# Kernel tuning notes

Hardware: AMD Instinct MI355X
Metric: run time of the kernel (lower is better)

The kernel has to match this reference:

```python
import jax, jax.numpy as jnp
import numpy as np

SQRT_D_K = 64 ** 0.5  # d_model ** 0.5 from __init__
NEG_INF = -1e9


def setup_inputs() -> dict:
    key = jax.random.key(0)
    kq, kk, kv, kp = jax.random.split(key, 4)
    B, H, S, Dh = 4, 16, 2048, 64
    q = jax.random.normal(kq, (B, H, S, Dh), dtype=jnp.float32)
    k = jax.random.normal(kk, (B, H, S, Dh), dtype=jnp.float32)
    v = jax.random.normal(kv, (B, H, S, Dh), dtype=jnp.float32)
    # causal mask: 1 above the diagonal (positions to mask), [1,1,S,S]
    casual_mask = jnp.triu(jnp.ones((S, S), dtype=jnp.int32), k=1)[None, None]
    # padding mask: 1 marks padded tokens, [B,S]
    padding_mask = jax.random.randint(kp, (B, S), 0, 2, dtype=jnp.int32)
    return {"q": q, "k": k, "v": v, "casual_mask": casual_mask,
            "padding_mask": padding_mask}


def reference(q, k, v, casual_mask, padding_mask):
    # score: [B,H,S,S]
    score = jnp.einsum("bhqd,bhkd->bhqk", q, k) / SQRT_D_K
    score = jnp.where(casual_mask == 1, NEG_INF, score)
    score = jnp.where(padding_mask[:, None, None, :] == 1, NEG_INF, score)
    attn_weights = jax.nn.softmax(score, axis=-1)
    # dropout p=0.0 (eval) -> identity
    attention_output = jnp.einsum("bhqk,bhkd->bhqd", attn_weights, v)
    return attention_output, attn_weights
```

## Files before the change

kernel.cpp:

```cpp
#include <hip/hip_runtime.h>
#include <hip/hip_bf16.h>

#define S_LEN 2048
#define DH    64
#define QT    128
#define KT    64
#define NW    4

typedef __attribute__((ext_vector_type(8))) short bf16x8;
typedef __attribute__((ext_vector_type(4))) float f32x4;
typedef __attribute__((ext_vector_type(4))) unsigned u32x4;
typedef __attribute__((ext_vector_type(2))) unsigned u32x2;

static __device__ __forceinline__ unsigned cvtpk(float a, float b) {
    unsigned r;
    asm("v_cvt_pk_bf16_f32 %0, %1, %2" : "=v"(r) : "v"(a), "v"(b));
    return r;
}

__global__ __launch_bounds__(256) void attn_main(
    const float* __restrict__ Q, const float* __restrict__ K,
    const float* __restrict__ V, const int* __restrict__ PAD,
    float* __restrict__ OUT, float* __restrict__ W)
{
    __shared__ short Kt[KT][72];
    __shared__ short VT[DH][72];
    __shared__ short Pb[NW][16][72];
    __shared__ float sinv[2][NW][16];
    __shared__ unsigned long long padm[32];

    const int orig = blockIdx.x;
    const int wg   = (orig & 7) * 128 + (orig >> 3);
    const int bh   = wg >> 4;
    const int qt   = 15 - (wg & 15);
    const int b    = bh >> 4;
    const int q0   = qt * QT;

    const int tid  = threadIdx.x;
    const int wv   = tid >> 6;
    const int l    = tid & 63;
    const int lr   = l & 15;
    const int lg   = l >> 4;
    const int k2   = (tid & 31) * 2;
    const int dblk = (tid >> 5) * 8;

    const size_t hoff = (size_t)bh * S_LEN * DH;
    const float* Qh = Q + hoff;
    const float* Kh = K + hoff;
    const float* Vh = V + hoff;
    float* Oh = OUT + hoff;
    float* Wh = W + (size_t)bh * S_LEN * S_LEN;

    const int nkt    = 2 * qt + 2;
    const int ktmaxA = 2 * qt;

    for (int i = tid; i < S_LEN; i += 256) {
        unsigned long long m = __ballot(PAD[b * S_LEN + i] != 0);
        if (l == 0) padm[i >> 6] = m;
    }

    bf16x8 qfA[2], qfB[2];
    #pragma unroll
    for (int blk = 0; blk < 2; ++blk) {
        const float* qp = Qh + (size_t)(q0 + blk * 64 + wv * 16 + lr) * DH + lg * 8;
        #pragma unroll
        for (int h = 0; h < 2; ++h) {
            f32x4 a  = *reinterpret_cast<const f32x4*>(qp + h * 32);
            f32x4 b4 = *reinterpret_cast<const f32x4*>(qp + h * 32 + 4);
            u32x4 t;
            t[0] = cvtpk(a[0] * 0.125f,  a[1] * 0.125f);
            t[1] = cvtpk(a[2] * 0.125f,  a[3] * 0.125f);
            t[2] = cvtpk(b4[0] * 0.125f, b4[1] * 0.125f);
            t[3] = cvtpk(b4[2] * 0.125f, b4[3] * 0.125f);
            (blk ? qfB[h] : qfA[h]) = __builtin_bit_cast(bf16x8, t);
        }
    }

    const f32x4 z4 = {0.f, 0.f, 0.f, 0.f};
    f32x4 accA[4] = {z4, z4, z4, z4};
    f32x4 accB[4] = {z4, z4, z4, z4};
    float rsA = 0.f, rsB = 0.f;
    const int qcolA = q0 + wv * 16 + lr;
    const int qcolB = qcolA + 64;

    auto ablock = [&](const bf16x8 (&qf)[2], const int qcol, float& rsref,
                      f32x4 (&accb)[4], const unsigned long long pm, const int ktbase) {
        f32x4 sc[4] = {z4, z4, z4, z4};
        #pragma unroll
        for (int s = 0; s < 4; ++s)
            #pragma unroll
            for (int h = 0; h < 2; ++h) {
                bf16x8 kf = *reinterpret_cast<const bf16x8*>(&Kt[s * 16 + lr][h * 32 + lg * 8]);
                sc[s] = __builtin_amdgcn_mfma_f32_16x16x32_bf16(kf, qf[h], sc[s], 0, 0, 0);
            }
        #pragma unroll
        for (int s = 0; s < 4; ++s) {
            const int kbase = ktbase + s * 16 + lg * 4;
            float e[4];
            #pragma unroll
            for (int r = 0; r < 4; ++r) {
                const bool padded = (pm >> (s * 16 + lg * 4 + r)) & 1ull;
                const bool ok = (kbase + r <= qcol) && !padded;
                e[r] = ok ? __expf(sc[s][r]) : 0.f;
                rsref += e[r];
            }
            u32x2 p2 = { cvtpk(e[0], e[1]), cvtpk(e[2], e[3]) };
            *reinterpret_cast<u32x2*>(&Pb[wv][lr][s * 16 + lg * 4]) = p2;
        }
        #pragma unroll
        for (int kk = 0; kk < 2; ++kk) {
            bf16x8 pf = *reinterpret_cast<const bf16x8*>(&Pb[wv][lr][kk * 32 + lg * 8]);
            #pragma unroll
            for (int dt = 0; dt < 4; ++dt) {
                bf16x8 vf = *reinterpret_cast<const bf16x8*>(&VT[dt * 16 + lr][kk * 32 + lg * 8]);
                accb[dt] = __builtin_amdgcn_mfma_f32_16x16x32_bf16(pf, vf, accb[dt], 0, 0, 0);
            }
        }
    };

    for (int kt = 0; kt < nkt; ++kt) {
        __syncthreads();
        {
            const float* kp = Kh + ((size_t)(kt * KT) + l) * DH + wv * 16;
            f32x4 pk0 = *reinterpret_cast<const f32x4*>(kp);
            f32x4 pk1 = *reinterpret_cast<const f32x4*>(kp + 4);
            f32x4 pk2 = *reinterpret_cast<const f32x4*>(kp + 8);
            f32x4 pk3 = *reinterpret_cast<const f32x4*>(kp + 12);
            const float* vp = Vh + ((size_t)(kt * KT) + k2) * DH + dblk;
            f32x4 pva0 = *reinterpret_cast<const f32x4*>(vp);
            f32x4 pva1 = *reinterpret_cast<const f32x4*>(vp + 4);
            f32x4 pvb0 = *reinterpret_cast<const f32x4*>(vp + DH);
            f32x4 pvb1 = *reinterpret_cast<const f32x4*>(vp + DH + 4);
            u32x4 ta, tb;
            ta[0] = cvtpk(pk0[0], pk0[1]); ta[1] = cvtpk(pk0[2], pk0[3]);
            ta[2] = cvtpk(pk1[0], pk1[1]); ta[3] = cvtpk(pk1[2], pk1[3]);
            tb[0] = cvtpk(pk2[0], pk2[1]); tb[1] = cvtpk(pk2[2], pk2[3]);
            tb[2] = cvtpk(pk3[0], pk3[1]); tb[3] = cvtpk(pk3[2], pk3[3]);
            *reinterpret_cast<u32x4*>(&Kt[l][wv * 16])     = ta;
            *reinterpret_cast<u32x4*>(&Kt[l][wv * 16 + 8]) = tb;
            #pragma unroll
            for (int j = 0; j < 4; ++j)
                *reinterpret_cast<unsigned*>(&VT[dblk + j][k2])     = cvtpk(pva0[j], pvb0[j]);
            #pragma unroll
            for (int j = 0; j < 4; ++j)
                *reinterpret_cast<unsigned*>(&VT[dblk + 4 + j][k2]) = cvtpk(pva1[j], pvb1[j]);
        }
        __syncthreads();

        const unsigned long long pm = padm[kt];
        if (kt <= ktmaxA) ablock(qfA, qcolA, rsA, accA, pm, kt * KT);
        ablock(qfB, qcolB, rsB, accB, pm, kt * KT);

        #pragma unroll 1
        for (int row = kt; row < QT; row += nkt) {
            const int kend = q0 + (row < 64 ? 64 : 128);
            const int n4 = (S_LEN - kend) >> 2;
            f32x4* dst = reinterpret_cast<f32x4*>(Wh + (size_t)(q0 + row) * S_LEN + kend);
            for (int i = tid; i < n4; i += 256)
                __builtin_nontemporal_store(z4, dst + i);
        }
    }

    rsA += __shfl_xor(rsA, 16, 64); rsA += __shfl_xor(rsA, 32, 64);
    rsB += __shfl_xor(rsB, 16, 64); rsB += __shfl_xor(rsB, 32, 64);
    const float invA = rsA > 0.f ? 1.f / rsA : 0.f;
    const float invB = rsB > 0.f ? 1.f / rsB : 0.f;

    if (lg == 0) { sinv[0][wv][lr] = invA; sinv[1][wv][lr] = invB; }
    float inv4A[4], inv4B[4];
    #pragma unroll
    for (int r = 0; r < 4; ++r) {
        inv4A[r] = sinv[0][wv][lg * 4 + r];
        inv4B[r] = sinv[1][wv][lg * 4 + r];
    }

    const int qa = q0 + wv * 16 + lg * 4;
    #pragma unroll
    for (int dt = 0; dt < 4; ++dt)
        #pragma unroll
        for (int r = 0; r < 4; ++r) {
            Oh[(size_t)(qa + r) * DH + dt * 16 + lr]      = accA[dt][r] * inv4A[r];
            Oh[(size_t)(qa + 64 + r) * DH + dt * 16 + lr] = accB[dt][r] * inv4B[r];
        }

    auto wblock = [&](const bf16x8 (&qf)[2], const int qcol, const float inv,
                      const unsigned long long pm, const int ktbase) {
        f32x4 sc[4] = {z4, z4, z4, z4};
        #pragma unroll
        for (int s = 0; s < 4; ++s)
            #pragma unroll
            for (int h = 0; h < 2; ++h) {
                bf16x8 kf = *reinterpret_cast<const bf16x8*>(&Kt[s * 16 + lr][h * 32 + lg * 8]);
                sc[s] = __builtin_amdgcn_mfma_f32_16x16x32_bf16(kf, qf[h], sc[s], 0, 0, 0);
            }
        #pragma unroll
        for (int s = 0; s < 4; ++s) {
            const int kbase = ktbase + s * 16 + lg * 4;
            f32x4 t;
            #pragma unroll
            for (int r = 0; r < 4; ++r) {
                const bool padded = (pm >> (s * 16 + lg * 4 + r)) & 1ull;
                const bool ok = (kbase + r <= qcol) && !padded;
                t[r] = ok ? __expf(sc[s][r]) * inv : 0.f;
            }
            __builtin_nontemporal_store(t,
                reinterpret_cast<f32x4*>(Wh + (size_t)qcol * S_LEN + kbase));
        }
    };

    for (int kt = 0; kt < nkt; ++kt) {
        __syncthreads();
        {
            const float* kp = Kh + ((size_t)(kt * KT) + l) * DH + wv * 16;
            f32x4 pk0 = *reinterpret_cast<const f32x4*>(kp);
            f32x4 pk1 = *reinterpret_cast<const f32x4*>(kp + 4);
            f32x4 pk2 = *reinterpret_cast<const f32x4*>(kp + 8);
            f32x4 pk3 = *reinterpret_cast<const f32x4*>(kp + 12);
            u32x4 ta, tb;
            ta[0] = cvtpk(pk0[0], pk0[1]); ta[1] = cvtpk(pk0[2], pk0[3]);
            ta[2] = cvtpk(pk1[0], pk1[1]); ta[3] = cvtpk(pk1[2], pk1[3]);
            tb[0] = cvtpk(pk2[0], pk2[1]); tb[1] = cvtpk(pk2[2], pk2[3]);
            tb[2] = cvtpk(pk3[0], pk3[1]); tb[3] = cvtpk(pk3[2], pk3[3]);
            *reinterpret_cast<u32x4*>(&Kt[l][wv * 16])     = ta;
            *reinterpret_cast<u32x4*>(&Kt[l][wv * 16 + 8]) = tb;
        }
        __syncthreads();

        const unsigned long long pm = padm[kt];
        if (kt <= ktmaxA) wblock(qfA, qcolA, invA, pm, kt * KT);
        wblock(qfB, qcolB, invB, pm, kt * KT);
    }
}

__global__ __launch_bounds__(256) void attn_fixup(
    const int* __restrict__ PAD, const float* __restrict__ V,
    float* __restrict__ OUT, float* __restrict__ W)
{
    const int bh = blockIdx.x;
    const int b  = bh >> 4;
    const int tid = threadIdx.x;
    __shared__ int red;
    __shared__ float tmp[256];
    __shared__ float vs[DH];
    if (tid == 0) red = S_LEN;
    __syncthreads();
    int m = S_LEN;
    for (int i = tid; i < S_LEN; i += 256)
        if (PAD[b * S_LEN + i] == 0) m = min(m, i);
    atomicMin(&red, m);
    __syncthreads();
    const int fz = red;
    if (fz == 0) return;

    const float* Vh = V + (size_t)bh * S_LEN * DH;
    float a = 0.f;
    const int dcol = tid & 63, part = tid >> 6;
    for (int kk = part; kk < S_LEN; kk += 4) a += Vh[(size_t)kk * DH + dcol];
    tmp[tid] = a;
    __syncthreads();
    if (tid < DH)
        vs[tid] = (tmp[tid] + tmp[tid + 64] + tmp[tid + 128] + tmp[tid + 192]) * (1.f / S_LEN);
    __syncthreads();

    float* Wh = W + (size_t)bh * S_LEN * S_LEN;
    float* Oh = OUT + (size_t)bh * S_LEN * DH;
    const f32x4 u = {1.f / S_LEN, 1.f / S_LEN, 1.f / S_LEN, 1.f / S_LEN};
    for (int qa2 = 0; qa2 < fz; ++qa2) {
        f32x4* dst = reinterpret_cast<f32x4*>(Wh + (size_t)qa2 * S_LEN);
        for (int i = tid; i < S_LEN / 4; i += 256) dst[i] = u;
        if (tid < DH) Oh[(size_t)qa2 * DH + tid] = vs[tid];
    }
}

extern "C" void kernel_launch(void* const* d_in, const int* in_sizes, int n_in,
                              void* d_out, int out_size, void* d_ws, size_t ws_size,
                              hipStream_t stream) {
    const float* q   = (const float*)d_in[0];
    const float* k   = (const float*)d_in[1];
    const float* v   = (const float*)d_in[2];
    const int*   pad = (const int*)d_in[4];

    float* out = (float*)d_out;
    float* w   = out + (size_t)4 * 16 * S_LEN * DH;

    attn_main<<<dim3(64 * 16), dim3(256), 0, stream>>>(q, k, v, pad, out, w);
    attn_fixup<<<dim3(64), dim3(256), 0, stream>>>(pad, v, out, w);
}
```

Before: 470.5 us.

## Split attention into rowsum kernel and fused PV-plus-weights kernel

Splits the single kernel into two launches. The first computes QK^T, the masked exp row sums and their inverses, and zero-fills the masked region of the weight matrix, writing the inverses to the workspace. The second recomputes scores and writes the normalized weights while it accumulates P·V in the same pass. This drops the separate second K pass inside one block and the V work from the rowsum stage, at the cost of an extra kernel launch and global round-trips for the inverse sums.

```diff
diff --git a/kernel.cpp b/kernel.cpp
--- a/kernel.cpp
+++ b/kernel.cpp
@@ -18,15 +18,12 @@
     return r;
 }
 
-__global__ __launch_bounds__(256) void attn_main(
+
+__global__ __launch_bounds__(256) void attn_rowsum(
     const float* __restrict__ Q, const float* __restrict__ K,
-    const float* __restrict__ V, const int* __restrict__ PAD,
-    float* __restrict__ OUT, float* __restrict__ W)
+    const int* __restrict__ PAD, float* __restrict__ W, float* __restrict__ INV)
 {
     __shared__ short Kt[KT][72];
-    __shared__ short VT[DH][72];
-    __shared__ short Pb[NW][16][72];
-    __shared__ float sinv[2][NW][16];
     __shared__ unsigned long long padm[32];
 
     const int orig = blockIdx.x;
@@ -36,19 +33,15 @@
     const int b    = bh >> 4;
     const int q0   = qt * QT;
 
-    const int tid  = threadIdx.x;
-    const int wv   = tid >> 6;
-    const int l    = tid & 63;
-    const int lr   = l & 15;
-    const int lg   = l >> 4;
-    const int k2   = (tid & 31) * 2;
-    const int dblk = (tid >> 5) * 8;
+    const int tid = threadIdx.x;
+    const int wv  = tid >> 6;
+    const int l   = tid & 63;
+    const int lr  = l & 15;
+    const int lg  = l >> 4;
 
     const size_t hoff = (size_t)bh * S_LEN * DH;
     const float* Qh = Q + hoff;
     const float* Kh = K + hoff;
-    const float* Vh = V + hoff;
-    float* Oh = OUT + hoff;
     float* Wh = W + (size_t)bh * S_LEN * S_LEN;
 
     const int nkt    = 2 * qt + 2;
@@ -77,14 +70,12 @@
     }
 
     const f32x4 z4 = {0.f, 0.f, 0.f, 0.f};
-    f32x4 accA[4] = {z4, z4, z4, z4};
-    f32x4 accB[4] = {z4, z4, z4, z4};
     float rsA = 0.f, rsB = 0.f;
     const int qcolA = q0 + wv * 16 + lr;
     const int qcolB = qcolA + 64;
 
-    auto ablock = [&](const bf16x8 (&qf)[2], const int qcol, float& rsref,
-                      f32x4 (&accb)[4], const unsigned long long pm, const int ktbase) {
+    auto rblock = [&](const bf16x8 (&qf)[2], const int qcol, float& rsref,
+                      const unsigned long long pm, const int ktbase) {
         f32x4 sc[4] = {z4, z4, z4, z4};
         #pragma unroll
         for (int s = 0; s < 4; ++s)
@@ -96,14 +87,144 @@
         #pragma unroll
         for (int s = 0; s < 4; ++s) {
             const int kbase = ktbase + s * 16 + lg * 4;
+            #pragma unroll
+            for (int r = 0; r < 4; ++r) {
+                const bool padded = (pm >> (s * 16 + lg * 4 + r)) & 1ull;
+                const bool ok = (kbase + r <= qcol) && !padded;
+                rsref += ok ? __expf(sc[s][r]) : 0.f;
+            }
+        }
+    };
+
+    for (int kt = 0; kt < nkt; ++kt) {
+        __syncthreads();
+        {
+            const float* kp = Kh + ((size_t)(kt * KT) + l) * DH + wv * 16;
+            f32x4 pk0 = *reinterpret_cast<const f32x4*>(kp);
+            f32x4 pk1 = *reinterpret_cast<const f32x4*>(kp + 4);
+            f32x4 pk2 = *reinterpret_cast<const f32x4*>(kp + 8);
+            f32x4 pk3 = *reinterpret_cast<const f32x4*>(kp + 12);
+            u32x4 ta, tb;
+            ta[0] = cvtpk(pk0[0], pk0[1]); ta[1] = cvtpk(pk0[2], pk0[3]);
+            ta[2] = cvtpk(pk1[0], pk1[1]); ta[3] = cvtpk(pk1[2], pk1[3]);
+            tb[0] = cvtpk(pk2[0], pk2[1]); tb[1] = cvtpk(pk2[2], pk2[3]);
+            tb[2] = cvtpk(pk3[0], pk3[1]); tb[3] = cvtpk(pk3[2], pk3[3]);
+            *reinterpret_cast<u32x4*>(&Kt[l][wv * 16])     = ta;
+            *reinterpret_cast<u32x4*>(&Kt[l][wv * 16 + 8]) = tb;
+        }
+        __syncthreads();
+
+        const unsigned long long pm = padm[kt];
+        if (kt <= ktmaxA) rblock(qfA, qcolA, rsA, pm, kt * KT);
+        rblock(qfB, qcolB, rsB, pm, kt * KT);
+
+        #pragma unroll 1
+        for (int row = kt; row < QT; row += nkt) {
+            const int kend = q0 + (row < 64 ? 64 : 128);
+            const int n4 = (S_LEN - kend) >> 2;
+            f32x4* dst = reinterpret_cast<f32x4*>(Wh + (size_t)(q0 + row) * S_LEN + kend);
+            for (int i = tid; i < n4; i += 256)
+                __builtin_nontemporal_store(z4, dst + i);
+        }
+    }
+
+    rsA += __shfl_xor(rsA, 16, 64); rsA += __shfl_xor(rsA, 32, 64);
+    rsB += __shfl_xor(rsB, 16, 64); rsB += __shfl_xor(rsB, 32, 64);
+    if (lg == 0) {
+        INV[(size_t)bh * S_LEN + qcolA] = rsA > 0.f ? 1.f / rsA : 0.f;
+        INV[(size_t)bh * S_LEN + qcolB] = rsB > 0.f ? 1.f / rsB : 0.f;
+    }
+}
+
+__global__ __launch_bounds__(256) void attn_fused(
+    const float* __restrict__ Q, const float* __restrict__ K,
+    const float* __restrict__ V, const int* __restrict__ PAD,
+    const float* __restrict__ INV, float* __restrict__ OUT, float* __restrict__ W)
+{
+    __shared__ short Kt[KT][72];
+    __shared__ short VT[DH][72];
+    __shared__ short Pb[NW][16][72];
+    __shared__ unsigned long long padm[32];
+
+    const int orig = blockIdx.x;
+    const int wg   = (orig & 7) * 128 + (orig >> 3);
+    const int bh   = wg >> 4;
+    const int qt   = 15 - (wg & 15);
+    const int b    = bh >> 4;
+    const int q0   = qt * QT;
+
+    const int tid  = threadIdx.x;
+    const int wv   = tid >> 6;
+    const int l    = tid & 63;
+    const int lr   = l & 15;
+    const int lg   = l >> 4;
+    const int k2   = (tid & 31) * 2;
+    const int dblk = (tid >> 5) * 8;
+
+    const size_t hoff = (size_t)bh * S_LEN * DH;
+    const float* Qh = Q + hoff;
+    const float* Kh = K + hoff;
+    const float* Vh = V + hoff;
+    float* Oh = OUT + hoff;
+    float* Wh = W + (size_t)bh * S_LEN * S_LEN;
+
+    const int nkt    = 2 * qt + 2;
+    const int ktmaxA = 2 * qt;
+
+    for (int i = tid; i < S_LEN; i += 256) {
+        unsigned long long m = __ballot(PAD[b * S_LEN + i] != 0);
+        if (l == 0) padm[i >> 6] = m;
+    }
+
+    bf16x8 qfA[2], qfB[2];
+    #pragma unroll
+    for (int blk = 0; blk < 2; ++blk) {
+        const float* qp = Qh + (size_t)(q0 + blk * 64 + wv * 16 + lr) * DH + lg * 8;
+        #pragma unroll
+        for (int h = 0; h < 2; ++h) {
+            f32x4 a  = *reinterpret_cast<const f32x4*>(qp + h * 32);
+            f32x4 b4 = *reinterpret_cast<const f32x4*>(qp + h * 32 + 4);
+            u32x4 t;
+            t[0] = cvtpk(a[0] * 0.125f,  a[1] * 0.125f);
+            t[1] = cvtpk(a[2] * 0.125f,  a[3] * 0.125f);
+            t[2] = cvtpk(b4[0] * 0.125f, b4[1] * 0.125f);
+            t[3] = cvtpk(b4[2] * 0.125f, b4[3] * 0.125f);
+            (blk ? qfB[h] : qfA[h]) = __builtin_bit_cast(bf16x8, t);
+        }
+    }
+
+    const f32x4 z4 = {0.f, 0.f, 0.f, 0.f};
+    f32x4 accA[4] = {z4, z4, z4, z4};
+    f32x4 accB[4] = {z4, z4, z4, z4};
+    const int qcolA = q0 + wv * 16 + lr;
+    const int qcolB = qcolA + 64;
+    const float invA = INV[(size_t)bh * S_LEN + qcolA];
+    const float invB = INV[(size_t)bh * S_LEN + qcolB];
+
+    auto fblock = [&](const bf16x8 (&qf)[2], const int qcol, const float inv,
+                      f32x4 (&accb)[4], const unsigned long long pm, const int ktbase) {
+        f32x4 sc[4] = {z4, z4, z4, z4};
+        #pragma unroll
+        for (int s = 0; s < 4; ++s)
+            #pragma unroll
+            for (int h = 0; h < 2; ++h) {
+                bf16x8 kf = *reinterpret_cast<const bf16x8*>(&Kt[s * 16 + lr][h * 32 + lg * 8]);
+                sc[s] = __builtin_amdgcn_mfma_f32_16x16x32_bf16(kf, qf[h], sc[s], 0, 0, 0);
+            }
+        #pragma unroll
+        for (int s = 0; s < 4; ++s) {
+            const int kbase = ktbase + s * 16 + lg * 4;
             float e[4];
+            f32x4 t;
             #pragma unroll
             for (int r = 0; r < 4; ++r) {
                 const bool padded = (pm >> (s * 16 + lg * 4 + r)) & 1ull;
                 const bool ok = (kbase + r <= qcol) && !padded;
                 e[r] = ok ? __expf(sc[s][r]) : 0.f;
-                rsref += e[r];
-            }
+                t[r] = e[r] * inv;
+            }
+            __builtin_nontemporal_store(t,
+                reinterpret_cast<f32x4*>(Wh + (size_t)qcol * S_LEN + kbase));
             u32x2 p2 = { cvtpk(e[0], e[1]), cvtpk(e[2], e[3]) };
             *reinterpret_cast<u32x2*>(&Pb[wv][lr][s * 16 + lg * 4]) = p2;
         }
@@ -148,33 +269,17 @@
         __syncthreads();
 
         const unsigned long long pm = padm[kt];
-        if (kt <= ktmaxA) ablock(qfA, qcolA, rsA, accA, pm, kt * KT);
-        ablock(qfB, qcolB, rsB, accB, pm, kt * KT);
-
-        #pragma unroll 1
-        for (int row = kt; row < QT; row += nkt) {
-            const int kend = q0 + (row < 64 ? 64 : 128);
-            const int n4 = (S_LEN - kend) >> 2;
-            f32x4* dst = reinterpret_cast<f32x4*>(Wh + (size_t)(q0 + row) * S_LEN + kend);
-            for (int i = tid; i < n4; i += 256)
-                __builtin_nontemporal_store(z4, dst + i);
-        }
-    }
-
-    rsA += __shfl_xor(rsA, 16, 64); rsA += __shfl_xor(rsA, 32, 64);
-    rsB += __shfl_xor(rsB, 16, 64); rsB += __shfl_xor(rsB, 32, 64);
-    const float invA = rsA > 0.f ? 1.f / rsA : 0.f;
-    const float invB = rsB > 0.f ? 1.f / rsB : 0.f;
-
-    if (lg == 0) { sinv[0][wv][lr] = invA; sinv[1][wv][lr] = invB; }
+        if (kt <= ktmaxA) fblock(qfA, qcolA, invA, accA, pm, kt * KT);
+        fblock(qfB, qcolB, invB, accB, pm, kt * KT);
+    }
+
+    const int qa = q0 + wv * 16 + lg * 4;
     float inv4A[4], inv4B[4];
     #pragma unroll
     for (int r = 0; r < 4; ++r) {
-        inv4A[r] = sinv[0][wv][lg * 4 + r];
-        inv4B[r] = sinv[1][wv][lg * 4 + r];
-    }
-
-    const int qa = q0 + wv * 16 + lg * 4;
+        inv4A[r] = INV[(size_t)bh * S_LEN + qa + r];
+        inv4B[r] = INV[(size_t)bh * S_LEN + qa + 64 + r];
+    }
     #pragma unroll
     for (int dt = 0; dt < 4; ++dt)
         #pragma unroll
@@ -182,54 +287,6 @@
             Oh[(size_t)(qa + r) * DH + dt * 16 + lr]      = accA[dt][r] * inv4A[r];
             Oh[(size_t)(qa + 64 + r) * DH + dt * 16 + lr] = accB[dt][r] * inv4B[r];
         }
-
-    auto wblock = [&](const bf16x8 (&qf)[2], const int qcol, const float inv,
-                      const unsigned long long pm, const int ktbase) {
-        f32x4 sc[4] = {z4, z4, z4, z4};
-        #pragma unroll
-        for (int s = 0; s < 4; ++s)
-            #pragma unroll
-            for (int h = 0; h < 2; ++h) {
-                bf16x8 kf = *reinterpret_cast<const bf16x8*>(&Kt[s * 16 + lr][h * 32 + lg * 8]);
-                sc[s] = __builtin_amdgcn_mfma_f32_16x16x32_bf16(kf, qf[h], sc[s], 0, 0, 0);
-            }
-        #pragma unroll
-        for (int s = 0; s < 4; ++s) {
-            const int kbase = ktbase + s * 16 + lg * 4;
-            f32x4 t;
-            #pragma unroll
-            for (int r = 0; r < 4; ++r) {
-                const bool padded = (pm >> (s * 16 + lg * 4 + r)) & 1ull;
-                const bool ok = (kbase + r <= qcol) && !padded;
-                t[r] = ok ? __expf(sc[s][r]) * inv : 0.f;
-            }
-            __builtin_nontemporal_store(t,
-                reinterpret_cast<f32x4*>(Wh + (size_t)qcol * S_LEN + kbase));
-        }
-    };
-
-    for (int kt = 0; kt < nkt; ++kt) {
-        __syncthreads();
-        {
-            const float* kp = Kh + ((size_t)(kt * KT) + l) * DH + wv * 16;
-            f32x4 pk0 = *reinterpret_cast<const f32x4*>(kp);
-            f32x4 pk1 = *reinterpret_cast<const f32x4*>(kp + 4);
-            f32x4 pk2 = *reinterpret_cast<const f32x4*>(kp + 8);
-            f32x4 pk3 = *reinterpret_cast<const f32x4*>(kp + 12);
-            u32x4 ta, tb;
-            ta[0] = cvtpk(pk0[0], pk0[1]); ta[1] = cvtpk(pk0[2], pk0[3]);
-            ta[2] = cvtpk(pk1[0], pk1[1]); ta[3] = cvtpk(pk1[2], pk1[3]);
-            tb[0] = cvtpk(pk2[0], pk2[1]); tb[1] = cvtpk(pk2[2], pk2[3]);
-            tb[2] = cvtpk(pk3[0], pk3[1]); tb[3] = cvtpk(pk3[2], pk3[3]);
-            *reinterpret_cast<u32x4*>(&Kt[l][wv * 16])     = ta;
-            *reinterpret_cast<u32x4*>(&Kt[l][wv * 16 + 8]) = tb;
-        }
-        __syncthreads();
-
-        const unsigned long long pm = padm[kt];
-        if (kt <= ktmaxA) wblock(qfA, qcolA, invA, pm, kt * KT);
-        wblock(qfB, qcolB, invB, pm, kt * KT);
-    }
 }
 
 __global__ __launch_bounds__(256) void attn_fixup(
@@ -282,7 +339,9 @@
 
     float* out = (float*)d_out;
     float* w   = out + (size_t)4 * 16 * S_LEN * DH;
-
-    attn_main<<<dim3(64 * 16), dim3(256), 0, stream>>>(q, k, v, pad, out, w);
+    float* inv = (float*)d_ws;
+
+    attn_rowsum<<<dim3(64 * 16), dim3(256), 0, stream>>>(q, k, pad, w, inv);
+    attn_fused<<<dim3(64 * 16), dim3(256), 0, stream>>>(q, k, v, pad, inv, out, w);
     attn_fixup<<<dim3(64), dim3(256), 0, stream>>>(pad, v, out, w);
 }
```

After: 500.5 us. 1.06x slower.
